# Performance work log

Measured on AMD Instinct MI355X. Metric: run time of the kernel, lower is better.

Reference implementation:

```python
import jax, jax.numpy as jnp
import numpy as np

# Module hyperparameters (match init_kwargs)
T0, Z0, T1, Z1, K, S, ROUTING = 4, 16, 8, 16, 5, 1, 3
PAD = 2  # hard-coded padding=2 in the torch module
N, H, W_SP = 4, 128, 128


def setup_inputs() -> dict:
    key = jax.random.key(0)
    k1, k2 = jax.random.split(key)
    u = jax.random.normal(k1, (N, T0, Z0, H, W_SP), dtype=jnp.float32)
    # t_0 independent Conv2d(z_0 -> t_1*z_1, k, s, padding=2, bias=False) weights
    W = jax.random.normal(k2, (T0, T1 * Z1, Z0, K, K), dtype=jnp.float32) * 0.05
    return {"u": u, "W": W}


def _squash(p):
    # squash along last (z_1) axis, matching torch: p_norm = sqrt(|p|^2 + 1e-9)
    n2 = jnp.sum(p * p, axis=-1, keepdims=True)
    n = jnp.sqrt(n2 + 1e-9)
    return n2 / (1.0 + n2) * p / n


def _capsule_convs(u, W):
    # t_0 independent convs == one grouped conv with feature_group_count=t_0
    n, t0, z0, h, w = u.shape
    x = u.reshape(n, t0 * z0, h, w)
    wk = W.reshape(t0 * T1 * Z1, z0, K, K)
    y = jax.lax.conv_general_dilated(
        x, wk, window_strides=(S, S), padding=[(PAD, PAD), (PAD, PAD)],
        dimension_numbers=("NCHW", "OIHW", "NCHW"), feature_group_count=t0)
    h1, w1 = y.shape[2], y.shape[3]
    # [N, t0*t1*z1, H1, W1] -> u_hat [t0, N, H1, W1, t1, z1]
    y = y.reshape(n, t0, T1, Z1, h1, w1)
    return jnp.transpose(y, (1, 0, 4, 5, 2, 3))


def _routing(u_hat):
    t0, n, h, w, t1, z1 = u_hat.shape
    dt = u_hat.dtype
    b = jnp.zeros((t0, n, t1, h, w), dt)  # NCHW layout per capsule type
    neg_inf = jnp.array(-jnp.inf, dt)
    zero = jnp.array(0.0, dt)
    win = (1, 1, 1, K, K)
    ones = (1, 1, 1, 1, 1)
    pad = [(0, 0), (0, 0), (0, 0), (PAD, PAD), (PAD, PAD)]
    v = None
    for d in range(ROUTING):
        uh = jax.lax.stop_gradient(u_hat) if d < ROUTING - 1 else u_hat
        # stability max: max_pool2d(k,1,pad=2) (pads with -inf) then max over t1
        b_max = jax.lax.reduce_window(b, neg_inf, jax.lax.max, win, ones, pad)
        b_max = jnp.max(b_max, axis=2, keepdims=True)
        c = jnp.exp(b - b_max)  # [t0, N, t1, H, W]
        # conv2d_same with ones kernel [1,t1,k,k] == channel-sum then kxk box-sum
        sum_c = jax.lax.reduce_window(jnp.sum(c, axis=2, keepdims=True), zero,
                                      jax.lax.add, win, ones, pad)
        r = c / sum_c                                   # [t0, N, t1, H, W]
        r = jnp.transpose(r, (0, 1, 3, 4, 2))[..., None]  # [t0,N,H,W,t1,1]
        p = jnp.sum(r * uh, axis=0)                     # [N, H, W, t1, z1]
        v = _squash(p)
        # NOTE: the original torch code computes b + (u_hat*v).sum(4) into a
        # list `b_t_list_` that is never assigned back, so b stays zero across
        # iterations. We faithfully reproduce that (no b update).
    return jnp.transpose(v, (0, 3, 4, 1, 2))  # [N, t1, z1, H, W]


def reference(u, W):
    return _routing(_capsule_convs(u, W))
```

## Files before the change

kernel.cpp:

```cpp
#include <hip/hip_runtime.h>
#include <hip/hip_bf16.h>


#define CI 64
#define CO 128

typedef __attribute__((ext_vector_type(8))) short bf16x8;
typedef __attribute__((ext_vector_type(4))) float f32x4;

__global__ __launch_bounds__(256) void k_reorder(const float* __restrict__ Wsrc,
                                                 ushort* __restrict__ Wr2) {
    int idx = blockIdx.x * 256 + threadIdx.x;
    if (idx >= 25 * 128 * 64) return;
    int ci = idx & 63;
    int r  = idx >> 6;
    int co = r & 127;
    int kk = r >> 7;
    int t0 = ci >> 4, z0 = ci & 15;
    __hip_bfloat16 b = __float2bfloat16(Wsrc[((t0 * CO + co) * 16 + z0) * 25 + kk]);
    Wr2[idx] = *(ushort*)&b;
}

__global__ __launch_bounds__(512) void k_caps(const float* __restrict__ u,
                                              const ushort* __restrict__ Wr2,
                                              float* __restrict__ out) {
    __shared__ ushort As[400 * 80];

    int tid = threadIdx.x;
    int bid = blockIdx.x;
    int bx = bid & 7, by = (bid >> 3) & 7, n = bid >> 6;
    int h0 = by * 16, w0 = bx * 16;

    const float* ub = u + (size_t)n * (CI * 128 * 128);

#pragma unroll
    for (int j = 0; j < 3; ++j) {
        int P = tid + j * 512;
        if (P < 1280) {
            int rr = P >> 6, ci = P & 63;
            int hh = h0 + rr - 2;
            bool rok = (unsigned)hh < 128u;
            const float* src = ub + (((size_t)ci << 7) + hh) * 128 + (w0 - 4);
            float4 ch[6];
#pragma unroll
            for (int k = 0; k < 6; ++k) {
                int wc = w0 - 4 + k * 4;
                ch[k] = (rok && (unsigned)wc < 128u)
                            ? *(const float4*)(src + k * 4)
                            : make_float4(0.f, 0.f, 0.f, 0.f);
            }
#pragma unroll
            for (int k = 0; k < 6; ++k) {
                float vals[4] = {ch[k].x, ch[k].y, ch[k].z, ch[k].w};
#pragma unroll
                for (int e = 0; e < 4; ++e) {
                    int cc = k * 4 + e - 2;
                    if ((unsigned)cc < 20u) {
                        __hip_bfloat16 bv = __float2bfloat16(vals[e]);
                        As[(rr * 20 + cc) * 80 + ci] = *(ushort*)&bv;
                    }
                }
            }
        }
    }
    __syncthreads();

    int lane = tid & 63, wid = tid >> 6;
    int wm = wid >> 2;
    int wn = wid & 3;
    int q = lane >> 4, m16 = lane & 15;

    f32x4 acc[8][2] = {};

    int aBase = (wm * 160 + m16) * 80 + q * 8;

    const ushort* bp = Wr2 + (wn * 32 + m16) * 64 + q * 8;
    bf16x8 bnxt0 = *(const bf16x8*)bp;
    bf16x8 bnxt1 = *(const bf16x8*)(bp + 1024);

    int soff = 0, kw = 0;
    for (int step = 0; step < 50; ++step) {
        int ks = step & 1;
        bf16x8 b0 = bnxt0, b1 = bnxt1;
        bp += ks ? (8192 - 32) : 32;
        if (step < 49) {
            bnxt0 = *(const bf16x8*)bp;
            bnxt1 = *(const bf16x8*)(bp + 1024);
        }
        int au = aBase + soff + ks * 32;
        bf16x8 a[8];
#pragma unroll
        for (int mi = 0; mi < 8; ++mi)
            a[mi] = *(const bf16x8*)(As + au + mi * 1600);
#pragma unroll
        for (int mi = 0; mi < 8; ++mi) {
            acc[mi][0] = __builtin_amdgcn_mfma_f32_16x16x32_bf16(a[mi], b0, acc[mi][0], 0, 0, 0);
            acc[mi][1] = __builtin_amdgcn_mfma_f32_16x16x32_bf16(a[mi], b1, acc[mi][1], 0, 0, 0);
        }
        if (ks) {
            if (kw < 4) { kw++; soff += 80; }
            else        { kw = 0; soff += 1280; }
        }
    }

#pragma unroll
    for (int mi = 0; mi < 8; ++mi) {
        int h = h0 + wm * 8 + mi;
        int hlo = h - 2; if (hlo < 0) hlo = 0;
        int hhi = h + 2; if (hhi > 127) hhi = 127;
        float cnth = (float)(hhi - hlo + 1);
#pragma unroll
        for (int ni = 0; ni < 2; ++ni) {
            f32x4 cv = acc[mi][ni];
            float ov[4];
#pragma unroll
            for (int reg = 0; reg < 4; ++reg) {
                int w = w0 + q * 4 + reg;
                int wlo = w - 2; if (wlo < 0) wlo = 0;
                int whi = w + 2; if (whi > 127) whi = 127;
                float s = 1.f / (8.f * cnth * (float)(whi - wlo + 1));
                float pv = cv[reg] * s;
                float n2 = pv * pv;
                n2 += __shfl_xor(n2, 1);
                n2 += __shfl_xor(n2, 2);
                n2 += __shfl_xor(n2, 4);
                n2 += __shfl_xor(n2, 8);
                float fac = n2 / ((1.f + n2) * sqrtf(n2 + 1e-9f));
                ov[reg] = pv * fac;
            }
            int co = wn * 32 + ni * 16 + m16;
            *(float4*)(out + (((size_t)(n * CO + co)) << 14) + h * 128 + w0 + q * 4) =
                make_float4(ov[0], ov[1], ov[2], ov[3]);
        }
    }
}

extern "C" void kernel_launch(void* const* d_in, const int* in_sizes, int n_in,
                              void* d_out, int out_size, void* d_ws, size_t ws_size,
                              hipStream_t stream) {
    const float* u    = (const float*)d_in[0];
    const float* Wsrc = (const float*)d_in[1];
    float* out = (float*)d_out;
    ushort* Wr2 = (ushort*)d_ws;

    k_reorder<<<800, 256, 0, stream>>>(Wsrc, Wr2);
    k_caps<<<256, 512, 0, stream>>>(u, Wr2, out);
}
```

Measured before the change: 118.5 us.

## Use 1024-thread blocks with 2x4 MFMA warp tiles and scalar-coalesced staging

Doubles the block size to 16 waves and re-tiles the MFMA work so each wave computes 2 row-tiles by 4 output-channel tiles instead of 8 by 2. More waves hide the latency of the per-step weight loads from global memory. The input staging becomes a scalar loop indexed along width for coalescing, and the LDS row stride drops from 80 to 72. In exchange each wave reuses A less and loads twice as many B fragments from global memory, and the scalar staging issues more load instructions. The 72-element stride may also change LDS bank conflicts.

```diff
diff --git a/kernel.cpp b/kernel.cpp
--- a/kernel.cpp
+++ b/kernel.cpp
@@ -2,7 +2,6 @@
 #include <hip/hip_bf16.h>
 
 
-#define CI 64
 #define CO 128
 
 typedef __attribute__((ext_vector_type(8))) short bf16x8;
@@ -21,96 +20,90 @@
     Wr2[idx] = *(ushort*)&b;
 }
 
-__global__ __launch_bounds__(512) void k_caps(const float* __restrict__ u,
-                                              const ushort* __restrict__ Wr2,
-                                              float* __restrict__ out) {
-    __shared__ ushort As[400 * 80];
+__global__ __launch_bounds__(1024) void k_caps(const float* __restrict__ u,
+                                               const ushort* __restrict__ Wr2,
+                                               float* __restrict__ out) {
+    __shared__ alignas(16) ushort As[400 * 72];
 
     int tid = threadIdx.x;
     int bid = blockIdx.x;
     int bx = bid & 7, by = (bid >> 3) & 7, n = bid >> 6;
     int h0 = by * 16, w0 = bx * 16;
 
-    const float* ub = u + (size_t)n * (CI * 128 * 128);
+    const float* ub = u + (size_t)n * (64 * 128 * 128);
 
-#pragma unroll
-    for (int j = 0; j < 3; ++j) {
-        int P = tid + j * 512;
-        if (P < 1280) {
-            int rr = P >> 6, ci = P & 63;
-            int hh = h0 + rr - 2;
-            bool rok = (unsigned)hh < 128u;
-            const float* src = ub + (((size_t)ci << 7) + hh) * 128 + (w0 - 4);
-            float4 ch[6];
-#pragma unroll
-            for (int k = 0; k < 6; ++k) {
-                int wc = w0 - 4 + k * 4;
-                ch[k] = (rok && (unsigned)wc < 128u)
-                            ? *(const float4*)(src + k * 4)
-                            : make_float4(0.f, 0.f, 0.f, 0.f);
-            }
-#pragma unroll
-            for (int k = 0; k < 6; ++k) {
-                float vals[4] = {ch[k].x, ch[k].y, ch[k].z, ch[k].w};
-#pragma unroll
-                for (int e = 0; e < 4; ++e) {
-                    int cc = k * 4 + e - 2;
-                    if ((unsigned)cc < 20u) {
-                        __hip_bfloat16 bv = __float2bfloat16(vals[e]);
-                        As[(rr * 20 + cc) * 80 + ci] = *(ushort*)&bv;
-                    }
-                }
-            }
-        }
+    for (int e = tid; e < 25600; e += 1024) {
+        int cc = e % 20;
+        int t  = e / 20;
+        int ci = t & 63;
+        int rr = t >> 6;
+        int hh = h0 + rr - 2, ww = w0 + cc - 2;
+        float v = 0.f;
+        if ((unsigned)hh < 128u && (unsigned)ww < 128u)
+            v = ub[((ci << 7) + hh) * 128 + ww];
+        __hip_bfloat16 bv = __float2bfloat16(v);
+        As[(rr * 20 + cc) * 72 + ci] = *(ushort*)&bv;
     }
     __syncthreads();
 
     int lane = tid & 63, wid = tid >> 6;
-    int wm = wid >> 2;
-    int wn = wid & 3;
+    int wm = wid >> 1;
+    int wn = wid & 1;
     int q = lane >> 4, m16 = lane & 15;
 
-    f32x4 acc[8][2] = {};
+    f32x4 acc[2][4] = {};
 
-    int aBase = (wm * 160 + m16) * 80 + q * 8;
+    int aB0 = ((wm * 2) * 20 + m16) * 72 + q * 8;
+    int aB1 = aB0 + 20 * 72;
 
-    const ushort* bp = Wr2 + (wn * 32 + m16) * 64 + q * 8;
-    bf16x8 bnxt0 = *(const bf16x8*)bp;
-    bf16x8 bnxt1 = *(const bf16x8*)(bp + 1024);
+    const ushort* bp = Wr2 + (wn * 64 + m16) * 64 + q * 8;
+    bf16x8 bn[4];
+#pragma unroll
+    for (int ni = 0; ni < 4; ++ni) bn[ni] = *(const bf16x8*)(bp + ni * 1024);
 
     int soff = 0, kw = 0;
-    for (int step = 0; step < 50; ++step) {
-        int ks = step & 1;
-        bf16x8 b0 = bnxt0, b1 = bnxt1;
-        bp += ks ? (8192 - 32) : 32;
-        if (step < 49) {
-            bnxt0 = *(const bf16x8*)bp;
-            bnxt1 = *(const bf16x8*)(bp + 1024);
+    for (int kk = 0; kk < 25; ++kk) {
+        bf16x8 bc[4], a0, a1;
+#pragma unroll
+        for (int ni = 0; ni < 4; ++ni) bc[ni] = bn[ni];
+#pragma unroll
+        for (int ni = 0; ni < 4; ++ni)
+            bn[ni] = *(const bf16x8*)(bp + 32 + ni * 1024);
+        a0 = *(const bf16x8*)(As + aB0 + soff);
+        a1 = *(const bf16x8*)(As + aB1 + soff);
+#pragma unroll
+        for (int ni = 0; ni < 4; ++ni) {
+            acc[0][ni] = __builtin_amdgcn_mfma_f32_16x16x32_bf16(a0, bc[ni], acc[0][ni], 0, 0, 0);
+            acc[1][ni] = __builtin_amdgcn_mfma_f32_16x16x32_bf16(a1, bc[ni], acc[1][ni], 0, 0, 0);
         }
-        int au = aBase + soff + ks * 32;
-        bf16x8 a[8];
 #pragma unroll
-        for (int mi = 0; mi < 8; ++mi)
-            a[mi] = *(const bf16x8*)(As + au + mi * 1600);
+        for (int ni = 0; ni < 4; ++ni) bc[ni] = bn[ni];
+        if (kk < 24) {
 #pragma unroll
-        for (int mi = 0; mi < 8; ++mi) {
-            acc[mi][0] = __builtin_amdgcn_mfma_f32_16x16x32_bf16(a[mi], b0, acc[mi][0], 0, 0, 0);
-            acc[mi][1] = __builtin_amdgcn_mfma_f32_16x16x32_bf16(a[mi], b1, acc[mi][1], 0, 0, 0);
+            for (int ni = 0; ni < 4; ++ni)
+                bn[ni] = *(const bf16x8*)(bp + 8192 + ni * 1024);
         }
-        if (ks) {
-            if (kw < 4) { kw++; soff += 80; }
-            else        { kw = 0; soff += 1280; }
+        a0 = *(const bf16x8*)(As + aB0 + soff + 32);
+        a1 = *(const bf16x8*)(As + aB1 + soff + 32);
+#pragma unroll
+        for (int ni = 0; ni < 4; ++ni) {
+            acc[0][ni] = __builtin_amdgcn_mfma_f32_16x16x32_bf16(a0, bc[ni], acc[0][ni], 0, 0, 0);
+            acc[1][ni] = __builtin_amdgcn_mfma_f32_16x16x32_bf16(a1, bc[ni], acc[1][ni], 0, 0, 0);
         }
+        bp += 8192;
+        bool roll = (kw == 4);
+        soff += roll ? 1152 : 72;
+        kw = roll ? 0 : kw + 1;
     }
 
 #pragma unroll
-    for (int mi = 0; mi < 8; ++mi) {
-        int h = h0 + wm * 8 + mi;
+    for (int mi = 0; mi < 2; ++mi) {
+        int h = h0 + wm * 2 + mi;
         int hlo = h - 2; if (hlo < 0) hlo = 0;
         int hhi = h + 2; if (hhi > 127) hhi = 127;
         float cnth = (float)(hhi - hlo + 1);
 #pragma unroll
-        for (int ni = 0; ni < 2; ++ni) {
+        for (int ni = 0; ni < 4; ++ni) {
             f32x4 cv = acc[mi][ni];
             float ov[4];
 #pragma unroll
@@ -128,7 +121,7 @@
                 float fac = n2 / ((1.f + n2) * sqrtf(n2 + 1e-9f));
                 ov[reg] = pv * fac;
             }
-            int co = wn * 32 + ni * 16 + m16;
+            int co = wn * 64 + ni * 16 + m16;
             *(float4*)(out + (((size_t)(n * CO + co)) << 14) + h * 128 + w0 + q * 4) =
                 make_float4(ov[0], ov[1], ov[2], ov[3]);
         }
@@ -144,5 +137,5 @@
     ushort* Wr2 = (ushort*)d_ws;
 
     k_reorder<<<800, 256, 0, stream>>>(Wsrc, Wr2);
-    k_caps<<<256, 512, 0, stream>>>(u, Wr2, out);
+    k_caps<<<256, 1024, 0, stream>>>(u, Wr2, out);
 }
```

Result: slower. 176.7 us (+49.1%).
